# Performance work log

Hardware: AMD Instinct MI355X
Metric: run time of the kernel (lower is better)

## Reference

```python
import jax, jax.numpy as jnp
import numpy as np

N, E, B = 50000, 800000, 64
D_IN, D_E = 192, 64
NUM_OUT = 256


def setup_inputs() -> dict:
    key = jax.random.key(0)
    ks = jax.random.split(key, 30)
    rn = lambda k, s: jax.random.normal(k, s, dtype=jnp.float32) * 0.05
    return {
        "x": jax.random.normal(ks[0], (N, D_IN), jnp.float32),
        "edge_index": jax.random.randint(ks[1], (2, E), 0, N, dtype=jnp.int32),
        "edge_attr": jax.random.normal(ks[2], (E, D_E), jnp.float32),
        "batch": jnp.sort(jax.random.randint(ks[3], (N,), 0, B, dtype=jnp.int32)),
        "W1": rn(ks[4], (D_IN, 256)), "as1": rn(ks[5], (4, 64)), "ad1": rn(ks[6], (4, 64)),
        "We1": rn(ks[7], (D_E, 256)), "ae1": rn(ks[8], (4, 64)), "b1": rn(ks[9], (256,)),
        "W2": rn(ks[10], (256, 256)), "as2": rn(ks[11], (4, 64)), "ad2": rn(ks[12], (4, 64)),
        "We2": rn(ks[13], (D_E, 256)), "ae2": rn(ks[14], (4, 64)), "b2": rn(ks[15], (256,)),
        "W3": rn(ks[16], (256, 512)), "as3": rn(ks[17], (4, 128)), "ad3": rn(ks[18], (4, 128)),
        "We3": rn(ks[19], (D_E, 512)), "ae3": rn(ks[20], (4, 128)), "b3": rn(ks[21], (128,)),
        "Wa": rn(ks[22], (128, NUM_OUT)), "ba": rn(ks[23], (NUM_OUT,)),
        "Wv": rn(ks[24], (128, 1)), "bv": rn(ks[25], (1,)),
    }


def reference(x, edge_index, edge_attr, batch,
              W1, as1, ad1, We1, ae1, b1,
              W2, as2, ad2, We2, ae2, b2,
              W3, as3, ad3, We3, ae3, b3,
              Wa, ba, Wv, bv):
    Nn = x.shape[0]
    src0, dst0 = edge_index[0], edge_index[1]
    # PyG add_self_loops(fill_value='mean'): self-loop edge_attr = mean of incoming edge_attr
    deg = jax.ops.segment_sum(jnp.ones_like(dst0, dtype=x.dtype), dst0, num_segments=Nn)
    loop_attr = jax.ops.segment_sum(edge_attr, dst0, num_segments=Nn) / jnp.maximum(deg, 1.0)[:, None]
    loop = jnp.arange(Nn, dtype=src0.dtype)
    src = jnp.concatenate([src0, loop])
    dst = jnp.concatenate([dst0, loop])
    ea = jnp.concatenate([edge_attr, loop_attr], axis=0)

    def gat(h, W, a_s, a_d, We, a_e, bias, concat):
        Hh, C = a_s.shape
        hs = (h @ W).reshape(Nn, Hh, C)                       # [N,H,C]
        al_s = (hs * a_s).sum(-1)                             # [N,H]
        al_d = (hs * a_d).sum(-1)                             # [N,H]
        al_e = ((ea @ We).reshape(-1, Hh, C) * a_e).sum(-1)   # [E+N,H]
        alpha = jax.nn.leaky_relu(al_s[src] + al_d[dst] + al_e, 0.2)
        amax = jax.ops.segment_max(alpha, dst, num_segments=Nn)
        w = jnp.exp(alpha - amax[dst])
        denom = jax.ops.segment_sum(w, dst, num_segments=Nn)
        w = w / (denom[dst] + 1e-16)                          # scatter-softmax over dst
        out = jax.ops.segment_sum(hs[src] * w[..., None], dst, num_segments=Nn)
        out = out.reshape(Nn, Hh * C) if concat else out.mean(axis=1)
        return out + bias

    h = jax.nn.relu(gat(x, W1, as1, ad1, We1, ae1, b1, True))
    h = jax.nn.relu(gat(h, W2, as2, ad2, We2, ae2, b2, True))
    h = gat(h, W3, as3, ad3, We3, ae3, b3, False)
    cnt = jax.ops.segment_sum(jnp.ones((Nn,), h.dtype), batch, num_segments=B)
    g = jax.ops.segment_sum(h, batch, num_segments=B) / jnp.maximum(cnt, 1.0)[:, None]
    logits = g @ Wa + ba
    value = g @ Wv + bv
    return jnp.concatenate([logits, value], axis=-1)  # [B, num_outputs+1]
```

## Files before the change

### kernel.cpp

```cpp
#include <hip/hip_runtime.h>
#include <hip/hip_bf16.h>


typedef __attribute__((ext_vector_type(8))) short short8;
typedef __attribute__((ext_vector_type(4))) float floatx4;

#define DEV __device__ __forceinline__

DEV unsigned short f2b(float f) {
  union { float f; unsigned u; } v; v.f = f;
  unsigned r = v.u + 0x7FFFu + ((v.u >> 16) & 1u);
  return (unsigned short)(r >> 16);
}
DEV float b2f(unsigned short u) {
  union { unsigned u; float f; } v; v.u = ((unsigned)u) << 16;
  return v.f;
}

__global__ void k_deg(const int* __restrict__ dst, int* __restrict__ deg, int E) {
  int e = blockIdx.x * 256 + threadIdx.x;
  if (e < E) atomicAdd(&deg[dst[e]], 1);
}

__global__ __launch_bounds__(256) void k_scan1(const int* __restrict__ deg,
    int* __restrict__ rowptr, int* __restrict__ bsum, int N) {
  __shared__ int sd[256];
  int b = blockIdx.x, tid = threadIdx.x;
  int i0 = b * 1024 + tid * 4;
  int v[4]; int s = 0;
#pragma unroll
  for (int j = 0; j < 4; j++) { int i = i0 + j; v[j] = (i < N) ? deg[i] : 0; s += v[j]; }
  sd[tid] = s;
  __syncthreads();
  for (int off = 1; off < 256; off <<= 1) {
    int t = (tid >= off) ? sd[tid - off] : 0;
    __syncthreads();
    sd[tid] += t;
    __syncthreads();
  }
  int run = sd[tid] - s;
#pragma unroll
  for (int j = 0; j < 4; j++) { int i = i0 + j; if (i < N) rowptr[i] = run; run += v[j]; }
  if (tid == 255) bsum[b] = sd[255];
}

__global__ __launch_bounds__(256) void k_scan2(int* __restrict__ bsum, int nb) {
  __shared__ int sd[256];
  int tid = threadIdx.x;
  int v = (tid < nb) ? bsum[tid] : 0;
  sd[tid] = v;
  __syncthreads();
  for (int off = 1; off < 256; off <<= 1) {
    int t = (tid >= off) ? sd[tid - off] : 0;
    __syncthreads();
    sd[tid] += t;
    __syncthreads();
  }
  if (tid < nb) bsum[tid] = sd[tid] - v;
}

__global__ __launch_bounds__(256) void k_scan3(int* __restrict__ rowptr,
    int* __restrict__ cursor, const int* __restrict__ bsum, int N, int E) {
  int b = blockIdx.x, tid = threadIdx.x;
  int add = bsum[b];
  int i0 = b * 1024 + tid * 4;
#pragma unroll
  for (int j = 0; j < 4; j++) {
    int i = i0 + j;
    if (i < N) { int r = rowptr[i] + add; rowptr[i] = r; cursor[i] = r; }
  }
  if (b == 0 && tid == 0) rowptr[N] = E;
}

__global__ void k_scatter(const int* __restrict__ src, const int* __restrict__ dst,
    int* __restrict__ cursor, int2* __restrict__ csr, int E) {
  int e = blockIdx.x * 256 + threadIdx.x;
  if (e < E) {
    int d = dst[e];
    int pos = atomicAdd(&cursor[d], 1);
    csr[pos] = make_int2(src[e], e);
  }
}

__global__ void k_wt(const float* __restrict__ W, unsigned short* __restrict__ Wt,
                     int K, int Nout) {
  int idx = blockIdx.x * 256 + threadIdx.x;
  if (idx < K * Nout) {
    int n = idx / K, k = idx - n * K;
    Wt[idx] = f2b(W[(size_t)k * Nout + n]);
  }
}

__global__ void k_wep(const float* __restrict__ We1, const float* __restrict__ ae1,
                      const float* __restrict__ We2, const float* __restrict__ ae2,
                      const float* __restrict__ We3, const float* __restrict__ ae3,
                      unsigned short* __restrict__ Wept) {
  int t = blockIdx.x * 256 + threadIdx.x;
  int j = t >> 6, c = t & 63;
  int L = j >> 2, h = j & 3;
  const float* We = (L == 0) ? We1 : (L == 1) ? We2 : We3;
  const float* ae = (L == 0) ? ae1 : (L == 1) ? ae2 : ae3;
  int C = (L == 2) ? 128 : 64;
  int HC = 4 * C;
  float s = 0.f;
  for (int cc = 0; cc < C; cc++) s += We[(size_t)c * HC + h * C + cc] * ae[h * C + cc];
  Wept[j * 64 + c] = f2b(s);
  if (t < 256) {
    int jj = 12 + (t >> 6);
    Wept[jj * 64 + (t & 63)] = 0;
  }
}

template<bool A_F32, int OUT_MODE, bool DO_ALD>
__global__ __launch_bounds__(256) void k_gemm(const void* __restrict__ Ap,
    const unsigned short* __restrict__ Bt, void* __restrict__ Cp,
    int M, int Nout, int K, int EN,
    const float* __restrict__ a_s, const float* __restrict__ a_d,
    float* __restrict__ als, float* __restrict__ ald) {
  __shared__ unsigned short As[64][40];
  __shared__ unsigned short Bs[64][40];
  const int tid = threadIdx.x;
  const int wave = tid >> 6, lane = tid & 63;
  const int quad = lane >> 4, l16 = lane & 15;
  const int m0 = blockIdx.x * 64, n0 = blockIdx.y * 64;
  const int arow = tid >> 2, acg = (tid & 3) * 8;
  floatx4 acc[4] = {{0,0,0,0},{0,0,0,0},{0,0,0,0},{0,0,0,0}};
  for (int k0 = 0; k0 < K; k0 += 32) {
    {
      int gm = m0 + arow;
      unsigned short tmp[8];
      if (A_F32) {
        const float* Af = (const float*)Ap;
        if (gm < M) {
          const float4* p = (const float4*)(Af + (size_t)gm * K + k0 + acg);
          float4 u0 = p[0], u1 = p[1];
          tmp[0]=f2b(u0.x); tmp[1]=f2b(u0.y); tmp[2]=f2b(u0.z); tmp[3]=f2b(u0.w);
          tmp[4]=f2b(u1.x); tmp[5]=f2b(u1.y); tmp[6]=f2b(u1.z); tmp[7]=f2b(u1.w);
        } else {
#pragma unroll
          for (int j = 0; j < 8; j++) tmp[j] = 0;
        }
      } else {
        const unsigned short* Ab = (const unsigned short*)Ap;
        uint4 u = {0,0,0,0};
        if (gm < M) u = *(const uint4*)(Ab + (size_t)gm * K + k0 + acg);
        *(uint4*)tmp = u;
      }
      *(uint4*)&As[arow][acg] = *(uint4*)tmp;
      int gn = n0 + arow;
      uint4 bv = {0,0,0,0};
      if (gn < Nout) bv = *(const uint4*)(Bt + (size_t)gn * K + k0 + acg);
      *(uint4*)&Bs[arow][acg] = bv;
    }
    __syncthreads();
    short8 a = *(const short8*)&As[wave * 16 + l16][quad * 8];
#pragma unroll
    for (int t = 0; t < 4; t++) {
      short8 b = *(const short8*)&Bs[t * 16 + l16][quad * 8];
      acc[t] = __builtin_amdgcn_mfma_f32_16x16x32_bf16(a, b, acc[t], 0, 0, 0);
    }
    __syncthreads();
  }
#pragma unroll
  for (int t = 0; t < 4; t++) {
#pragma unroll
    for (int r = 0; r < 4; r++) {
      int row = m0 + wave * 16 + quad * 4 + r;
      int col = n0 + t * 16 + l16;
      float v = acc[t][r];
      if (OUT_MODE == 0) {
        if (row < M && col < Nout)
          ((unsigned short*)Cp)[(size_t)row * Nout + col] = f2b(v);
      } else {
        if (row < M && col < 12)
          ((float*)Cp)[((size_t)(col >> 2) * EN + row) * 4 + (col & 3)] = v;
      }
    }
  }
  if constexpr (DO_ALD) {
    int h = (n0 * 4) / Nout;
#pragma unroll
    for (int r = 0; r < 4; r++) {
      float ps = 0.f, pd = 0.f;
#pragma unroll
      for (int t = 0; t < 4; t++) {
        int col = n0 + t * 16 + l16;
        float v = acc[t][r];
        ps += v * a_s[col];
        pd += v * a_d[col];
      }
#pragma unroll
      for (int off = 1; off < 16; off <<= 1) {
        ps += __shfl_xor(ps, off, 64);
        pd += __shfl_xor(pd, off, 64);
      }
      int row = m0 + wave * 16 + quad * 4 + r;
      if (l16 == 0 && row < M) {
        atomicAdd(&als[row * 4 + h], ps);
        atomicAdd(&ald[row * 4 + h], pd);
      }
    }
  }
}

__global__ void k_loop_ale(const int* __restrict__ rowptr, const int2* __restrict__ csr,
                           float* __restrict__ ale, int N, int E) {
  int n = blockIdx.x * 256 + threadIdx.x;
  if (n >= N) return;
  const size_t EN = (size_t)E + N;
  int s = rowptr[n], e = rowptr[n + 1];
  float a[12];
#pragma unroll
  for (int j = 0; j < 12; j++) a[j] = 0.f;
  for (int p = s; p < e; p++) {
    int eid = csr[p].y;
#pragma unroll
    for (int L = 0; L < 3; L++) {
      float4 v = *(const float4*)(ale + (L * EN + eid) * 4);
      a[L * 4 + 0] += v.x; a[L * 4 + 1] += v.y;
      a[L * 4 + 2] += v.z; a[L * 4 + 3] += v.w;
    }
  }
  float inv = 1.0f / (float)((e - s) > 1 ? (e - s) : 1);
#pragma unroll
  for (int L = 0; L < 3; L++)
    *(float4*)(ale + (L * EN + E + n) * 4) =
        make_float4(a[L*4+0]*inv, a[L*4+1]*inv, a[L*4+2]*inv, a[L*4+3]*inv);
}

template<int VPL, int MODE, int UF>
__global__ __launch_bounds__(256) void k_agg(const unsigned short* __restrict__ hs,
    const int* __restrict__ rowptr, const int2* __restrict__ csr,
    const float* __restrict__ ale,
    const float* __restrict__ als, const float* __restrict__ ald,
    const float* __restrict__ bias, unsigned short* __restrict__ outb,
    float* __restrict__ outf, int N, int E) {
  const int HC = 16 * VPL;
  __shared__ float s_w[4][4][16][4];
  __shared__ int   s_s[4][4][16];
  const int wave = threadIdx.x >> 6;
  const int lane = threadIdx.x & 63;
  const int grp  = lane >> 4;
  const int sl   = lane & 15;
  const int hd   = sl >> 2;
  const int node = blockIdx.x * 16 + wave * 4 + grp;
  if (node >= N) return;
  int start = rowptr[node];
  int cnt   = rowptr[node + 1] - start;
  int total = cnt + 1;
  const float4 aldv = *(const float4*)(ald + node * 4);
  float m0=-1e30f, m1=-1e30f, m2=-1e30f, m3=-1e30f;
  float d0=0.f, d1=0.f, d2=0.f, d3=0.f;
  float acc[VPL];
#pragma unroll
  for (int j = 0; j < VPL; j++) acc[j] = 0.f;
  for (int base = 0; base < total; base += 16) {
    int ei = base + sl;
    bool active = ei < total;
    float a0=-1e30f, a1=-1e30f, a2=-1e30f, a3=-1e30f;
    int sidx = node;
    if (active) {
      const float* alep;
      if (ei < cnt) {
        int2 se = csr[start + ei];
        sidx = se.x;
        alep = ale + (size_t)se.y * 4;
      } else {
        alep = ale + ((size_t)E + node) * 4;
      }
      float4 ev = *(const float4*)alep;
      float4 sv = *(const float4*)(als + sidx * 4);
      a0 = sv.x + aldv.x + ev.x;
      a1 = sv.y + aldv.y + ev.y;
      a2 = sv.z + aldv.z + ev.z;
      a3 = sv.w + aldv.w + ev.w;
      a0 = a0 > 0.f ? a0 : 0.2f * a0;
      a1 = a1 > 0.f ? a1 : 0.2f * a1;
      a2 = a2 > 0.f ? a2 : 0.2f * a2;
      a3 = a3 > 0.f ? a3 : 0.2f * a3;
    }
    float c0=a0, c1=a1, c2=a2, c3=a3;
#pragma unroll
    for (int off = 8; off > 0; off >>= 1) {
      c0 = fmaxf(c0, __shfl_xor(c0, off, 64));
      c1 = fmaxf(c1, __shfl_xor(c1, off, 64));
      c2 = fmaxf(c2, __shfl_xor(c2, off, 64));
      c3 = fmaxf(c3, __shfl_xor(c3, off, 64));
    }
    float n0v = fmaxf(m0, c0), n1v = fmaxf(m1, c1), n2v = fmaxf(m2, c2), n3v = fmaxf(m3, c3);
    float p0 = active ? __expf(a0 - n0v) : 0.f;
    float p1 = active ? __expf(a1 - n1v) : 0.f;
    float p2 = active ? __expf(a2 - n2v) : 0.f;
    float p3 = active ? __expf(a3 - n3v) : 0.f;
    float s0=p0, s1=p1, s2=p2, s3=p3;
#pragma unroll
    for (int off = 8; off > 0; off >>= 1) {
      s0 += __shfl_xor(s0, off, 64);
      s1 += __shfl_xor(s1, off, 64);
      s2 += __shfl_xor(s2, off, 64);
      s3 += __shfl_xor(s3, off, 64);
    }
    float r0 = __expf(m0 - n0v), r1 = __expf(m1 - n1v);
    float r2 = __expf(m2 - n2v), r3 = __expf(m3 - n3v);
    d0 = d0 * r0 + s0; d1 = d1 * r1 + s1; d2 = d2 * r2 + s2; d3 = d3 * r3 + s3;
    float rh = hd == 0 ? r0 : hd == 1 ? r1 : hd == 2 ? r2 : r3;
#pragma unroll
    for (int j = 0; j < VPL; j++) acc[j] *= rh;
    m0 = n0v; m1 = n1v; m2 = n2v; m3 = n3v;
    *(float4*)&s_w[wave][grp][sl][0] = make_float4(p0, p1, p2, p3);
    s_s[wave][grp][sl] = sidx;
    __threadfence_block();
    int chunk = total - base; if (chunk > 16) chunk = 16;
    int t = 0;
    for (; t + UF <= chunk; t += UF) {
      float w[UF]; int sp[UF];
#pragma unroll
      for (int u = 0; u < UF; u++) {
        w[u]  = s_w[wave][grp][t + u][hd];
        sp[u] = s_s[wave][grp][t + u];
      }
      unsigned short v[UF][VPL];
#pragma unroll
      for (int u = 0; u < UF; u++) {
        const unsigned short* p = hs + (size_t)sp[u] * HC + sl * VPL;
#pragma unroll
        for (int q = 0; q < VPL / 8; q++) ((uint4*)v[u])[q] = ((const uint4*)p)[q];
      }
#pragma unroll
      for (int u = 0; u < UF; u++) {
#pragma unroll
        for (int j = 0; j < VPL; j++) acc[j] += w[u] * b2f(v[u][j]);
      }
    }
    for (; t < chunk; t++) {
      float w0 = s_w[wave][grp][t][hd];
      int sp0 = s_s[wave][grp][t];
      const unsigned short* p = hs + (size_t)sp0 * HC + sl * VPL;
      unsigned short v0[VPL];
#pragma unroll
      for (int q = 0; q < VPL / 8; q++) ((uint4*)v0)[q] = ((const uint4*)p)[q];
#pragma unroll
      for (int j = 0; j < VPL; j++) acc[j] += w0 * b2f(v0[j]);
    }
  }
  float dh = hd == 0 ? d0 : hd == 1 ? d1 : hd == 2 ? d2 : d3;
  float inv = 1.0f / (dh + 1e-16f);
  if constexpr (MODE == 0) {
    unsigned short tmp[VPL];
#pragma unroll
    for (int j = 0; j < VPL; j++) {
      float v = acc[j] * inv + bias[sl * VPL + j];
      tmp[j] = f2b(fmaxf(v, 0.f));
    }
    unsigned short* op = outb + (size_t)node * HC + sl * VPL;
#pragma unroll
    for (int q = 0; q < VPL / 8; q++) ((uint4*)op)[q] = ((uint4*)tmp)[q];
  } else {
#pragma unroll
    for (int j = 0; j < VPL; j++) {
      float v = acc[j] * inv;
      v += __shfl_xor(v, 4, 64);
      v += __shfl_xor(v, 8, 64);
      acc[j] = v * 0.25f;
    }
    if (sl < 4) {
      float* op = outf + (size_t)node * (4 * VPL) + sl * VPL;
#pragma unroll
      for (int j = 0; j < VPL; j++) op[j] = acc[j] + bias[sl * VPL + j];
    }
  }
}

__global__ __launch_bounds__(256) void k_pool(const float* __restrict__ out3,
    const int* __restrict__ bat, float* __restrict__ g, int* __restrict__ cntb, int N) {
  int wid = blockIdx.x * 4 + (threadIdx.x >> 6);
  int lane = threadIdx.x & 63;
  int per = (N + 255) / 256;
  int s = wid * per, e = s + per;
  if (e > N) e = N;
  if (s >= e) return;
  int cur = bat[s];
  float ax = 0.f, ay = 0.f; int run = 0;
  for (int n = s; n < e; n++) {
    int b = bat[n];
    if (b != cur) {
      atomicAdd(&g[cur * 128 + lane * 2], ax);
      atomicAdd(&g[cur * 128 + lane * 2 + 1], ay);
      if (lane == 0) atomicAdd(&cntb[cur], run);
      ax = 0.f; ay = 0.f; run = 0; cur = b;
    }
    float2 v = *(const float2*)(out3 + (size_t)n * 128 + lane * 2);
    ax += v.x; ay += v.y; run++;
  }
  atomicAdd(&g[cur * 128 + lane * 2], ax);
  atomicAdd(&g[cur * 128 + lane * 2 + 1], ay);
  if (lane == 0) atomicAdd(&cntb[cur], run);
}

__global__ __launch_bounds__(320) void k_final(const float* __restrict__ g,
    const int* __restrict__ cntb, const float* __restrict__ Wa, const float* __restrict__ ba,
    const float* __restrict__ Wv, const float* __restrict__ bv, float* __restrict__ out) {
  __shared__ float gm[128];
  int b = blockIdx.x, t = threadIdx.x;
  if (t < 128) {
    float c = (float)cntb[b];
    gm[t] = g[b * 128 + t] / fmaxf(c, 1.f);
  }
  __syncthreads();
  if (t < 257) {
    float acc = 0.f;
    if (t < 256) {
      for (int k = 0; k < 128; k++) acc += gm[k] * Wa[k * 256 + t];
      acc += ba[t];
    } else {
      for (int k = 0; k < 128; k++) acc += gm[k] * Wv[k];
      acc += bv[0];
    }
    out[b * 257 + t] = acc;
  }
}

extern "C" void kernel_launch(void* const* d_in, const int* in_sizes, int n_in,
                              void* d_out, int out_size, void* d_ws, size_t ws_size,
                              hipStream_t stream) {
  const float* x   = (const float*)d_in[0];
  const int*   ei  = (const int*)  d_in[1];
  const float* ea  = (const float*)d_in[2];
  const int*   bat = (const int*)  d_in[3];
  const float* W1  = (const float*)d_in[4];
  const float* as1 = (const float*)d_in[5];
  const float* ad1 = (const float*)d_in[6];
  const float* We1 = (const float*)d_in[7];
  const float* ae1 = (const float*)d_in[8];
  const float* b1  = (const float*)d_in[9];
  const float* W2  = (const float*)d_in[10];
  const float* as2 = (const float*)d_in[11];
  const float* ad2 = (const float*)d_in[12];
  const float* We2 = (const float*)d_in[13];
  const float* ae2 = (const float*)d_in[14];
  const float* b2  = (const float*)d_in[15];
  const float* W3  = (const float*)d_in[16];
  const float* as3 = (const float*)d_in[17];
  const float* ad3 = (const float*)d_in[18];
  const float* We3 = (const float*)d_in[19];
  const float* ae3 = (const float*)d_in[20];
  const float* b3  = (const float*)d_in[21];
  const float* Wa  = (const float*)d_in[22];
  const float* ba  = (const float*)d_in[23];
  const float* Wv  = (const float*)d_in[24];
  const float* bv  = (const float*)d_in[25];
  (void)n_in; (void)out_size; (void)ws_size;

  const int N = in_sizes[0] / 192;
  const int E = in_sizes[1] / 2;
  const size_t EN = (size_t)E + N;
  const int* srcv = ei;
  const int* dstv = ei + E;
  const int nb = (N + 1023) / 1024;

  size_t off = 0;
  auto alloc = [&](size_t bytes) -> char* {
    char* p = (char*)d_ws + off;
    off += (bytes + 255) & ~(size_t)255;
    return p;
  };
  int* deg     = (int*)alloc((size_t)N * 4);
  int* rowptr  = (int*)alloc((size_t)(N + 1) * 4);
  int* cursor  = (int*)alloc((size_t)N * 4);
  int* bsum    = (int*)alloc(256 * 4);
  int2* csr    = (int2*)alloc((size_t)E * 8);
  float* ale   = (float*)alloc(3 * EN * 4 * 4);
  unsigned short* Wept = (unsigned short*)alloc(16 * 64 * 2);
  unsigned short* W1t  = (unsigned short*)alloc(256 * 192 * 2);
  unsigned short* W2t  = (unsigned short*)alloc(256 * 256 * 2);
  unsigned short* W3t  = (unsigned short*)alloc(512 * 256 * 2);
  unsigned short* hs   = (unsigned short*)alloc((size_t)N * 512 * 2);
  unsigned short* h1   = (unsigned short*)alloc((size_t)N * 256 * 2);
  unsigned short* h2   = (unsigned short*)alloc((size_t)N * 256 * 2);
  float* out3  = (float*)alloc((size_t)N * 128 * 4);
  float* als_all = (float*)alloc((size_t)N * 4 * 4 * 6);
  float* g     = (float*)alloc(64 * 128 * 4 + 64 * 4);
  int* cntb    = (int*)(g + 64 * 128);
  float* als1 = als_all + (size_t)N * 4 * 0;
  float* ald1 = als_all + (size_t)N * 4 * 1;
  float* als2 = als_all + (size_t)N * 4 * 2;
  float* ald2 = als_all + (size_t)N * 4 * 3;
  float* als3 = als_all + (size_t)N * 4 * 4;
  float* ald3 = als_all + (size_t)N * 4 * 5;

  hipMemsetAsync(deg, 0, (size_t)N * 4, stream);
  hipMemsetAsync(als_all, 0, (size_t)N * 4 * 4 * 6, stream);
  hipMemsetAsync(g, 0, 64 * 128 * 4 + 64 * 4, stream);

  k_deg<<<(E + 255) / 256, 256, 0, stream>>>(dstv, deg, E);
  k_scan1<<<nb, 256, 0, stream>>>(deg, rowptr, bsum, N);
  k_scan2<<<1, 256, 0, stream>>>(bsum, nb);
  k_scan3<<<nb, 256, 0, stream>>>(rowptr, cursor, bsum, N, E);
  k_scatter<<<(E + 255) / 256, 256, 0, stream>>>(srcv, dstv, cursor, csr, E);
  k_wt<<<(192 * 256 + 255) / 256, 256, 0, stream>>>(W1, W1t, 192, 256);
  k_wt<<<(256 * 256 + 255) / 256, 256, 0, stream>>>(W2, W2t, 256, 256);
  k_wt<<<(256 * 512 + 255) / 256, 256, 0, stream>>>(W3, W3t, 256, 512);
  k_wep<<<3, 256, 0, stream>>>(We1, ae1, We2, ae2, We3, ae3, Wept);
  k_gemm<true, 2, false><<<dim3((E + 63) / 64, 1), 256, 0, stream>>>(
      ea, Wept, ale, E, 16, 64, (int)EN, nullptr, nullptr, nullptr, nullptr);
  k_loop_ale<<<(N + 255) / 256, 256, 0, stream>>>(rowptr, csr, ale, N, E);
  k_gemm<true, 0, true><<<dim3((N + 63) / 64, 4), 256, 0, stream>>>(
      x, W1t, hs, N, 256, 192, 0, as1, ad1, als1, ald1);
  k_agg<16, 0, 4><<<(N + 15) / 16, 256, 0, stream>>>(
      hs, rowptr, csr, ale + 0 * EN * 4, als1, ald1, b1, h1, nullptr, N, E);
  k_gemm<false, 0, true><<<dim3((N + 63) / 64, 4), 256, 0, stream>>>(
      h1, W2t, hs, N, 256, 256, 0, as2, ad2, als2, ald2);
  k_agg<16, 0, 4><<<(N + 15) / 16, 256, 0, stream>>>(
      hs, rowptr, csr, ale + 1 * EN * 4, als2, ald2, b2, h2, nullptr, N, E);
  k_gemm<false, 0, true><<<dim3((N + 63) / 64, 8), 256, 0, stream>>>(
      h2, W3t, hs, N, 512, 256, 0, as3, ad3, als3, ald3);
  k_agg<32, 1, 2><<<(N + 15) / 16, 256, 0, stream>>>(
      hs, rowptr, csr, ale + 2 * EN * 4, als3, ald3, b3, nullptr, out3, N, E);
  k_pool<<<64, 256, 0, stream>>>(out3, bat, g, cntb, N);
  k_final<<<64, 320, 0, stream>>>(g, cntb, Wa, ba, Wv, bv, (float*)d_out);
}
```

Measured before the change: 1.059 ms.

## Restructure GAT aggregation: 8 lanes per node, prefetch next edge chunk

For the 256-wide layers, the aggregation kernel now maps each node to 8 lanes holding 32 features each, instead of 16 lanes of 16, so every block processes twice as many nodes. The next chunk's CSR entry, edge logit and source logit are loaded one iteration ahead so their latency overlaps the current gather. The gather loop issues two rows' 128-bit loads together and converts bf16 with bit masks. The costs are higher register pressure from 32 accumulators, which may lower occupancy, and fewer edges handled per chunk on the 256-wide layers.

After: 1.068 ms. Within noise of the previous version (+0.9%).

```diff
diff --git a/kernel.cpp b/kernel.cpp
--- a/kernel.cpp
+++ b/kernel.cpp
@@ -4,6 +4,7 @@
 
 typedef __attribute__((ext_vector_type(8))) short short8;
 typedef __attribute__((ext_vector_type(4))) float floatx4;
+typedef __attribute__((ext_vector_type(4))) unsigned int uintx4;
 
 #define DEV __device__ __forceinline__
 
@@ -228,52 +229,54 @@
         make_float4(a[L*4+0]*inv, a[L*4+1]*inv, a[L*4+2]*inv, a[L*4+3]*inv);
 }
 
-template<int VPL, int MODE, int UF>
+template<int LPN, int MODE>
 __global__ __launch_bounds__(256) void k_agg(const unsigned short* __restrict__ hs,
     const int* __restrict__ rowptr, const int2* __restrict__ csr,
     const float* __restrict__ ale,
     const float* __restrict__ als, const float* __restrict__ ald,
     const float* __restrict__ bias, unsigned short* __restrict__ outb,
     float* __restrict__ outf, int N, int E) {
-  const int HC = 16 * VPL;
-  __shared__ float s_w[4][4][16][4];
-  __shared__ int   s_s[4][4][16];
+  const int FPL = 32;
+  const int HC  = LPN * FPL;
+  const int NG  = 64 / LPN;
+  __shared__ float s_w[4][NG][LPN][4];
+  __shared__ int   s_s[4][NG][LPN];
   const int wave = threadIdx.x >> 6;
   const int lane = threadIdx.x & 63;
-  const int grp  = lane >> 4;
-  const int sl   = lane & 15;
-  const int hd   = sl >> 2;
-  const int node = blockIdx.x * 16 + wave * 4 + grp;
+  const int grp  = lane / LPN;
+  const int sl   = lane % LPN;
+  const int hd   = sl >> (LPN >> 3);
+  const int node = blockIdx.x * (4 * NG) + wave * NG + grp;
   if (node >= N) return;
   int start = rowptr[node];
   int cnt   = rowptr[node + 1] - start;
   int total = cnt + 1;
-  const float4 aldv = *(const float4*)(ald + node * 4);
+  const float4 aldv   = *(const float4*)(ald + (size_t)node * 4);
+  const float4 selfev = *(const float4*)(ale + ((size_t)E + node) * 4);
+  const float4 selfsv = *(const float4*)(als + (size_t)node * 4);
+  int    psidx = node;
+  float4 pev = selfev, psv = selfsv;
+  if (sl < cnt) {
+    int2 se = csr[start + sl];
+    psidx = se.x;
+    pev = *(const float4*)(ale + (size_t)se.y * 4);
+    psv = *(const float4*)(als + (size_t)se.x * 4);
+  }
   float m0=-1e30f, m1=-1e30f, m2=-1e30f, m3=-1e30f;
   float d0=0.f, d1=0.f, d2=0.f, d3=0.f;
-  float acc[VPL];
-#pragma unroll
-  for (int j = 0; j < VPL; j++) acc[j] = 0.f;
-  for (int base = 0; base < total; base += 16) {
+  float acc[FPL];
+#pragma unroll
+  for (int j = 0; j < FPL; j++) acc[j] = 0.f;
+  for (int base = 0; base < total; base += LPN) {
     int ei = base + sl;
     bool active = ei < total;
     float a0=-1e30f, a1=-1e30f, a2=-1e30f, a3=-1e30f;
-    int sidx = node;
+    int sidx = psidx;
     if (active) {
-      const float* alep;
-      if (ei < cnt) {
-        int2 se = csr[start + ei];
-        sidx = se.x;
-        alep = ale + (size_t)se.y * 4;
-      } else {
-        alep = ale + ((size_t)E + node) * 4;
-      }
-      float4 ev = *(const float4*)alep;
-      float4 sv = *(const float4*)(als + sidx * 4);
-      a0 = sv.x + aldv.x + ev.x;
-      a1 = sv.y + aldv.y + ev.y;
-      a2 = sv.z + aldv.z + ev.z;
-      a3 = sv.w + aldv.w + ev.w;
+      a0 = psv.x + aldv.x + pev.x;
+      a1 = psv.y + aldv.y + pev.y;
+      a2 = psv.z + aldv.z + pev.z;
+      a3 = psv.w + aldv.w + pev.w;
       a0 = a0 > 0.f ? a0 : 0.2f * a0;
       a1 = a1 > 0.f ? a1 : 0.2f * a1;
       a2 = a2 > 0.f ? a2 : 0.2f * a2;
@@ -281,7 +284,7 @@
     }
     float c0=a0, c1=a1, c2=a2, c3=a3;
 #pragma unroll
-    for (int off = 8; off > 0; off >>= 1) {
+    for (int off = LPN / 2; off > 0; off >>= 1) {
       c0 = fmaxf(c0, __shfl_xor(c0, off, 64));
       c1 = fmaxf(c1, __shfl_xor(c1, off, 64));
       c2 = fmaxf(c2, __shfl_xor(c2, off, 64));
@@ -294,7 +297,7 @@
     float p3 = active ? __expf(a3 - n3v) : 0.f;
     float s0=p0, s1=p1, s2=p2, s3=p3;
 #pragma unroll
-    for (int off = 8; off > 0; off >>= 1) {
+    for (int off = LPN / 2; off > 0; off >>= 1) {
       s0 += __shfl_xor(s0, off, 64);
       s1 += __shfl_xor(s1, off, 64);
       s2 += __shfl_xor(s2, off, 64);
@@ -305,68 +308,104 @@
     d0 = d0 * r0 + s0; d1 = d1 * r1 + s1; d2 = d2 * r2 + s2; d3 = d3 * r3 + s3;
     float rh = hd == 0 ? r0 : hd == 1 ? r1 : hd == 2 ? r2 : r3;
 #pragma unroll
-    for (int j = 0; j < VPL; j++) acc[j] *= rh;
+    for (int j = 0; j < FPL; j++) acc[j] *= rh;
     m0 = n0v; m1 = n1v; m2 = n2v; m3 = n3v;
     *(float4*)&s_w[wave][grp][sl][0] = make_float4(p0, p1, p2, p3);
     s_s[wave][grp][sl] = sidx;
     __threadfence_block();
-    int chunk = total - base; if (chunk > 16) chunk = 16;
+    if (base + LPN < total) {
+      int nei = base + LPN + sl;
+      psidx = node; pev = selfev; psv = selfsv;
+      if (nei < cnt) {
+        int2 se = csr[start + nei];
+        psidx = se.x;
+        pev = *(const float4*)(ale + (size_t)se.y * 4);
+        psv = *(const float4*)(als + (size_t)se.x * 4);
+      }
+    }
+    int chunk = total - base; if (chunk > LPN) chunk = LPN;
     int t = 0;
-    for (; t + UF <= chunk; t += UF) {
-      float w[UF]; int sp[UF];
-#pragma unroll
-      for (int u = 0; u < UF; u++) {
-        w[u]  = s_w[wave][grp][t + u][hd];
-        sp[u] = s_s[wave][grp][t + u];
-      }
-      unsigned short v[UF][VPL];
-#pragma unroll
-      for (int u = 0; u < UF; u++) {
-        const unsigned short* p = hs + (size_t)sp[u] * HC + sl * VPL;
-#pragma unroll
-        for (int q = 0; q < VPL / 8; q++) ((uint4*)v[u])[q] = ((const uint4*)p)[q];
-      }
-#pragma unroll
-      for (int u = 0; u < UF; u++) {
-#pragma unroll
-        for (int j = 0; j < VPL; j++) acc[j] += w[u] * b2f(v[u][j]);
-      }
-    }
-    for (; t < chunk; t++) {
+    for (; t + 2 <= chunk; t += 2) {
       float w0 = s_w[wave][grp][t][hd];
-      int sp0 = s_s[wave][grp][t];
-      const unsigned short* p = hs + (size_t)sp0 * HC + sl * VPL;
-      unsigned short v0[VPL];
-#pragma unroll
-      for (int q = 0; q < VPL / 8; q++) ((uint4*)v0)[q] = ((const uint4*)p)[q];
-#pragma unroll
-      for (int j = 0; j < VPL; j++) acc[j] += w0 * b2f(v0[j]);
+      float w1 = s_w[wave][grp][t + 1][hd];
+      int   q0 = s_s[wave][grp][t];
+      int   q1 = s_s[wave][grp][t + 1];
+      const uintx4* p0p = (const uintx4*)(hs + (size_t)q0 * HC + sl * FPL);
+      const uintx4* p1p = (const uintx4*)(hs + (size_t)q1 * HC + sl * FPL);
+      uintx4 v0[4], v1[4];
+#pragma unroll
+      for (int q = 0; q < 4; q++) v0[q] = p0p[q];
+#pragma unroll
+      for (int q = 0; q < 4; q++) v1[q] = p1p[q];
+      asm volatile("" :: "v"(v0[0]), "v"(v0[1]), "v"(v0[2]), "v"(v0[3]),
+                         "v"(v1[0]), "v"(v1[1]), "v"(v1[2]), "v"(v1[3]));
+#pragma unroll
+      for (int q = 0; q < 4; q++) {
+        uintx4 x = v0[q];
+#pragma unroll
+        for (int k = 0; k < 4; k++) {
+          float lo = __uint_as_float(x[k] << 16);
+          float hi = __uint_as_float(x[k] & 0xffff0000u);
+          acc[q * 8 + k * 2 + 0] += w0 * lo;
+          acc[q * 8 + k * 2 + 1] += w0 * hi;
+        }
+      }
+#pragma unroll
+      for (int q = 0; q < 4; q++) {
+        uintx4 x = v1[q];
+#pragma unroll
+        for (int k = 0; k < 4; k++) {
+          float lo = __uint_as_float(x[k] << 16);
+          float hi = __uint_as_float(x[k] & 0xffff0000u);
+          acc[q * 8 + k * 2 + 0] += w1 * lo;
+          acc[q * 8 + k * 2 + 1] += w1 * hi;
+        }
+      }
+    }
+    if (t < chunk) {
+      float w0 = s_w[wave][grp][t][hd];
+      int   q0 = s_s[wave][grp][t];
+      const uintx4* p0p = (const uintx4*)(hs + (size_t)q0 * HC + sl * FPL);
+      uintx4 v0[4];
+#pragma unroll
+      for (int q = 0; q < 4; q++) v0[q] = p0p[q];
+#pragma unroll
+      for (int q = 0; q < 4; q++) {
+        uintx4 x = v0[q];
+#pragma unroll
+        for (int k = 0; k < 4; k++) {
+          float lo = __uint_as_float(x[k] << 16);
+          float hi = __uint_as_float(x[k] & 0xffff0000u);
+          acc[q * 8 + k * 2 + 0] += w0 * lo;
+          acc[q * 8 + k * 2 + 1] += w0 * hi;
+        }
+      }
     }
   }
   float dh = hd == 0 ? d0 : hd == 1 ? d1 : hd == 2 ? d2 : d3;
   float inv = 1.0f / (dh + 1e-16f);
   if constexpr (MODE == 0) {
-    unsigned short tmp[VPL];
-#pragma unroll
-    for (int j = 0; j < VPL; j++) {
-      float v = acc[j] * inv + bias[sl * VPL + j];
+    unsigned short tmp[FPL];
+#pragma unroll
+    for (int j = 0; j < FPL; j++) {
+      float v = acc[j] * inv + bias[sl * FPL + j];
       tmp[j] = f2b(fmaxf(v, 0.f));
     }
-    unsigned short* op = outb + (size_t)node * HC + sl * VPL;
-#pragma unroll
-    for (int q = 0; q < VPL / 8; q++) ((uint4*)op)[q] = ((uint4*)tmp)[q];
+    unsigned short* op = outb + (size_t)node * HC + sl * FPL;
+#pragma unroll
+    for (int q = 0; q < 4; q++) ((uint4*)op)[q] = ((uint4*)tmp)[q];
   } else {
 #pragma unroll
-    for (int j = 0; j < VPL; j++) {
+    for (int j = 0; j < FPL; j++) {
       float v = acc[j] * inv;
       v += __shfl_xor(v, 4, 64);
       v += __shfl_xor(v, 8, 64);
       acc[j] = v * 0.25f;
     }
     if (sl < 4) {
-      float* op = outf + (size_t)node * (4 * VPL) + sl * VPL;
-#pragma unroll
-      for (int j = 0; j < VPL; j++) op[j] = acc[j] + bias[sl * VPL + j];
+      float* op = outf + (size_t)node * (4 * FPL) + sl * FPL;
+#pragma unroll
+      for (int j = 0; j < FPL; j++) op[j] = acc[j] + bias[sl * FPL + j];
     }
   }
 }
@@ -506,15 +545,15 @@
   k_loop_ale<<<(N + 255) / 256, 256, 0, stream>>>(rowptr, csr, ale, N, E);
   k_gemm<true, 0, true><<<dim3((N + 63) / 64, 4), 256, 0, stream>>>(
       x, W1t, hs, N, 256, 192, 0, as1, ad1, als1, ald1);
-  k_agg<16, 0, 4><<<(N + 15) / 16, 256, 0, stream>>>(
+  k_agg<8, 0><<<(N + 31) / 32, 256, 0, stream>>>(
       hs, rowptr, csr, ale + 0 * EN * 4, als1, ald1, b1, h1, nullptr, N, E);
   k_gemm<false, 0, true><<<dim3((N + 63) / 64, 4), 256, 0, stream>>>(
       h1, W2t, hs, N, 256, 256, 0, as2, ad2, als2, ald2);
-  k_agg<16, 0, 4><<<(N + 15) / 16, 256, 0, stream>>>(
+  k_agg<8, 0><<<(N + 31) / 32, 256, 0, stream>>>(
       hs, rowptr, csr, ale + 1 * EN * 4, als2, ald2, b2, h2, nullptr, N, E);
   k_gemm<false, 0, true><<<dim3((N + 63) / 64, 8), 256, 0, stream>>>(
       h2, W3t, hs, N, 512, 256, 0, as3, ad3, als3, ald3);
-  k_agg<32, 1, 2><<<(N + 15) / 16, 256, 0, stream>>>(
+  k_agg<16, 1><<<(N + 15) / 16, 256, 0, stream>>>(
       hs, rowptr, csr, ale + 2 * EN * 4, als3, ald3, b3, nullptr, out3, N, E);
   k_pool<<<64, 256, 0, stream>>>(out3, bat, g, cntb, N);
   k_final<<<64, 320, 0, stream>>>(g, cntb, Wa, ba, Wv, bv, (float*)d_out);
```
